# Optimization experiments

Hardware: AMD Instinct MI355X
Metric: run time of the kernel (lower is better)

The kernel has to match this reference:

```python
import jax, jax.numpy as jnp
import numpy as np

N_NODES = 100000
N_EDGES = 1600000
DIM = 64


def setup_inputs() -> dict:
    key = jax.random.key(0)
    k = jax.random.split(key, 7)
    x = jax.random.normal(k[0], (N_NODES, DIM), dtype=jnp.float32)
    edge_index = jax.random.randint(k[1], (2, N_EDGES), 0, N_NODES, dtype=jnp.int64)
    sim_weight = jax.random.uniform(k[2], (N_EDGES,), dtype=jnp.float32)
    rep = jax.random.normal(k[3], (N_NODES,), dtype=jnp.float32)
    node_signal = jax.random.uniform(k[4], (N_NODES,), dtype=jnp.float32)
    # xavier-normal-ish linear weights, stored as [in, out] for x @ W
    std = float(np.sqrt(2.0 / (DIM + DIM)))
    W = jax.random.normal(k[5], (DIM, DIM), dtype=jnp.float32) * std
    W_self = jax.random.normal(k[6], (DIM, DIM), dtype=jnp.float32) * std
    return {"x": x, "edge_index": edge_index, "sim_weight": sim_weight,
            "rep": rep, "node_signal": node_signal, "W": W, "W_self": W_self}


def reference(x, edge_index, sim_weight, rep, node_signal, W, W_self):
    row, col = edge_index[0], edge_index[1]
    n = x.shape[0]
    hx = x @ W                                   # [N, D]
    h_j = hx[col]                                # [E, D] gather
    gate = jax.nn.sigmoid(rep[row] + rep[col])   # [E]
    coef = sim_weight * gate * node_signal[col]  # [E] fused edge scalar
    msg = coef[:, None] * h_j                    # [E, D]
    out = jax.ops.segment_sum(msg, row, num_segments=n)              # [N, D]
    deg = jax.ops.segment_sum(jnp.ones_like(row, dtype=x.dtype), row,
                              num_segments=n)                        # [N]
    out = out / (deg[:, None] + 1e-6)
    out = out + jax.nn.sigmoid(rep)[:, None] * (x @ W_self)
    return jax.nn.leaky_relu(out, negative_slope=0.01)
```

## Files before the change

### kernel.cpp

```cpp
#include <hip/hip_runtime.h>
#include <math.h>

#define DIM 64
#define R_SHIFT 7
#define R_PART  128
#define CHUNK   2048
#define EPT     4
#define CAP     4096
#define PCAP    3072

static __device__ inline unsigned short f32_to_bf16(float f) {
    unsigned u = __float_as_uint(f);
    u += 0x7FFFu + ((u >> 16) & 1u);
    return (unsigned short)(u >> 16);
}
static __device__ inline float bf16_to_f32(unsigned short h) {
    return __uint_as_float((unsigned)h << 16);
}

static __device__ inline unsigned pack_entry(int c, float coef) {
    unsigned u = __float_as_uint(coef);
    u += 0x7FFFu + ((u >> 16) & 1u);
    unsigned cb = (u >> 16) & 0x7FFFu;
    return ((unsigned)c << 15) | cb;
}
static __device__ inline int entry_col(unsigned e) { return (int)(e >> 15); }
static __device__ inline float entry_coef(unsigned e) {
    return __uint_as_float((e & 0x7FFFu) << 16);
}

__global__ __launch_bounds__(256) void gemm_dual_tiled(
        const float* __restrict__ x,
        const float* __restrict__ W,
        const float* __restrict__ Wself,
        const float* __restrict__ rep,
        unsigned short* __restrict__ hxb,
        unsigned short* __restrict__ selfb, int n) {
    __shared__ float xs[64][68];
    __shared__ float Ws[64][64];
    __shared__ float Vs[64][64];

    const int t = threadIdx.x;
    const int row0 = blockIdx.x * 64;

    {
        const float4* W4 = (const float4*)W;
        const float4* V4 = (const float4*)Wself;
        float4* Ws4 = (float4*)&Ws[0][0];
        float4* Vs4 = (float4*)&Vs[0][0];
        for (int i = t; i < 1024; i += 256) { Ws4[i] = W4[i]; Vs4[i] = V4[i]; }
    }
    for (int i = t; i < 1024; i += 256) {
        int r = i >> 4, c4 = i & 15;
        float4 v = make_float4(0.f, 0.f, 0.f, 0.f);
        if (row0 + r < n) v = ((const float4*)x)[(size_t)(row0 + r) * 16 + c4];
        *(float4*)&xs[r][c4 * 4] = v;
    }
    __syncthreads();

    const int r0 = (t >> 4) * 4;
    const int c0 = (t & 15) * 4;

    float4 a1[4], a2[4];
#pragma unroll
    for (int j = 0; j < 4; ++j) {
        a1[j] = make_float4(0.f, 0.f, 0.f, 0.f);
        a2[j] = make_float4(0.f, 0.f, 0.f, 0.f);
    }

#pragma unroll 8
    for (int k = 0; k < 64; ++k) {
        float4 wv = *(const float4*)&Ws[k][c0];
        float4 vv = *(const float4*)&Vs[k][c0];
        float xk0 = xs[r0 + 0][k];
        float xk1 = xs[r0 + 1][k];
        float xk2 = xs[r0 + 2][k];
        float xk3 = xs[r0 + 3][k];

        a1[0].x = fmaf(xk0, wv.x, a1[0].x); a1[0].y = fmaf(xk0, wv.y, a1[0].y);
        a1[0].z = fmaf(xk0, wv.z, a1[0].z); a1[0].w = fmaf(xk0, wv.w, a1[0].w);
        a1[1].x = fmaf(xk1, wv.x, a1[1].x); a1[1].y = fmaf(xk1, wv.y, a1[1].y);
        a1[1].z = fmaf(xk1, wv.z, a1[1].z); a1[1].w = fmaf(xk1, wv.w, a1[1].w);
        a1[2].x = fmaf(xk2, wv.x, a1[2].x); a1[2].y = fmaf(xk2, wv.y, a1[2].y);
        a1[2].z = fmaf(xk2, wv.z, a1[2].z); a1[2].w = fmaf(xk2, wv.w, a1[2].w);
        a1[3].x = fmaf(xk3, wv.x, a1[3].x); a1[3].y = fmaf(xk3, wv.y, a1[3].y);
        a1[3].z = fmaf(xk3, wv.z, a1[3].z); a1[3].w = fmaf(xk3, wv.w, a1[3].w);

        a2[0].x = fmaf(xk0, vv.x, a2[0].x); a2[0].y = fmaf(xk0, vv.y, a2[0].y);
        a2[0].z = fmaf(xk0, vv.z, a2[0].z); a2[0].w = fmaf(xk0, vv.w, a2[0].w);
        a2[1].x = fmaf(xk1, vv.x, a2[1].x); a2[1].y = fmaf(xk1, vv.y, a2[1].y);
        a2[1].z = fmaf(xk1, vv.z, a2[1].z); a2[1].w = fmaf(xk1, vv.w, a2[1].w);
        a2[2].x = fmaf(xk2, vv.x, a2[2].x); a2[2].y = fmaf(xk2, vv.y, a2[2].y);
        a2[2].z = fmaf(xk2, vv.z, a2[2].z); a2[2].w = fmaf(xk2, vv.w, a2[2].w);
        a2[3].x = fmaf(xk3, vv.x, a2[3].x); a2[3].y = fmaf(xk3, vv.y, a2[3].y);
        a2[3].z = fmaf(xk3, vv.z, a2[3].z); a2[3].w = fmaf(xk3, vv.w, a2[3].w);
    }

#pragma unroll
    for (int j = 0; j < 4; ++j) {
        int row = row0 + r0 + j;
        if (row >= n) break;
        ushort4 hb;
        hb.x = f32_to_bf16(a1[j].x); hb.y = f32_to_bf16(a1[j].y);
        hb.z = f32_to_bf16(a1[j].z); hb.w = f32_to_bf16(a1[j].w);
        *(ushort4*)&hxb[(size_t)row * DIM + c0] = hb;
        float srep = 1.0f / (1.0f + __expf(-rep[row]));
        ushort4 sb;
        sb.x = f32_to_bf16(srep * a2[j].x); sb.y = f32_to_bf16(srep * a2[j].y);
        sb.z = f32_to_bf16(srep * a2[j].z); sb.w = f32_to_bf16(srep * a2[j].w);
        *(ushort4*)&selfb[(size_t)row * DIM + c0] = sb;
    }
}

__global__ __launch_bounds__(512) void ppart_kernel(
        const int* __restrict__ ei,
        const float* __restrict__ sw,
        const float* __restrict__ rep,
        const float* __restrict__ ns,
        int* __restrict__ pcur,
        uint2* __restrict__ tmp, int E, int NP) {
    __shared__ int cnt[1024];
    __shared__ int gb[1024];
    for (int p = threadIdx.x; p < NP; p += 512) cnt[p] = 0;
    __syncthreads();

    const int base = blockIdx.x * CHUNK;

    int r_[EPT], c_[EPT]; float sw_[EPT];
#pragma unroll
    for (int i = 0; i < EPT; ++i) {
        int e = base + i * 512 + threadIdx.x;
        bool v = (e < E);
        r_[i]  = v ? ei[e] : -1;
        c_[i]  = v ? ei[E + e] : 0;
        sw_[i] = v ? sw[e] : 0.f;
    }

    float repr[EPT], repc[EPT], nsc[EPT];
#pragma unroll
    for (int i = 0; i < EPT; ++i) {
        int rr = (r_[i] >= 0) ? r_[i] : 0;
        int cc = c_[i];
        repr[i] = rep[rr];
        repc[i] = rep[cc];
        nsc[i]  = ns[cc];
    }

    int pid[EPT]; int rank[EPT]; unsigned pay[EPT];
#pragma unroll
    for (int i = 0; i < EPT; ++i) {
        pid[i] = -1;
        if (r_[i] >= 0) {
            float gate = 1.0f / (1.0f + __expf(-(repr[i] + repc[i])));
            float coef = sw_[i] * gate * nsc[i];
            pid[i]  = r_[i] >> R_SHIFT;
            pay[i]  = pack_entry(c_[i], coef);
            rank[i] = atomicAdd(&cnt[pid[i]], 1);
        }
    }
    __syncthreads();

    for (int p = threadIdx.x; p < NP; p += 512) {
        int c = cnt[p];
        gb[p] = c ? atomicAdd(&pcur[p], c) : 0;
    }
    __syncthreads();

#pragma unroll
    for (int i = 0; i < EPT; ++i)
        if (pid[i] >= 0) {
            int s = gb[pid[i]] + rank[i];
            if (s < PCAP)
                tmp[(size_t)pid[i] * PCAP + s] = make_uint2((unsigned)r_[i], pay[i]);
        }
}

template<int K>
__device__ inline void lgather_k(const unsigned* __restrict__ sorted, int j,
                                 const unsigned short* __restrict__ hxb,
                                 int lane, float& acc) {
    unsigned e[K]; unsigned short h[K];
#pragma unroll
    for (int i = 0; i < K; ++i) e[i] = sorted[j + i];
#pragma unroll
    for (int i = 0; i < K; ++i) h[i] = hxb[(size_t)entry_col(e[i]) * DIM + lane];
#pragma unroll
    for (int i = 0; i < K; ++i) acc = fmaf(entry_coef(e[i]), bf16_to_f32(h[i]), acc);
}

__global__ __launch_bounds__(512) void pgather2_kernel(
        const int* __restrict__ pcur,
        const uint2* __restrict__ tmp,
        const unsigned short* __restrict__ hxb,
        const unsigned short* __restrict__ selfb,
        float* __restrict__ out, int n) {
    __shared__ unsigned sorted[CAP];
    __shared__ int rbase[R_PART + 1];
    __shared__ int rcnt[R_PART];
    __shared__ int rcur[R_PART];

    const int p   = blockIdx.x;
    const int tid = threadIdx.x;
    const size_t start = (size_t)p * PCAP;
    int cnt = pcur[p];
    if (cnt > PCAP) cnt = PCAP;

    if (tid < R_PART) rcnt[tid] = 0;
    __syncthreads();

    for (int i = tid; i < cnt; i += 512)
        atomicAdd(&rcnt[tmp[start + i].x & (R_PART - 1)], 1);
    __syncthreads();

    if (tid < 64) {
        int c0 = rcnt[2 * tid], c1 = rcnt[2 * tid + 1];
        int s = c0 + c1;
        int inc = s;
#pragma unroll
        for (int off = 1; off < 64; off <<= 1) {
            int t = __shfl_up(inc, off, 64);
            if (tid >= off) inc += t;
        }
        int excl = inc - s;
        rbase[2 * tid]     = excl;
        rbase[2 * tid + 1] = excl + c0;
        rcur[2 * tid]      = excl;
        rcur[2 * tid + 1]  = excl + c0;
        if (tid == 63) rbase[R_PART] = inc;
    }
    __syncthreads();

    for (int i = tid; i < cnt; i += 512) {
        uint2 t = tmp[start + i];
        int slot = atomicAdd(&rcur[t.x & (R_PART - 1)], 1);
        sorted[slot] = t.y;
    }
    __syncthreads();

    const int lane = tid & 63;
    const int w    = tid >> 6;
    const int gbase = p << R_SHIFT;
    for (int r = w; r < R_PART; r += 8) {
        int g = gbase + r;
        if (g >= n) continue;
        const int b0 = rbase[r], b1 = rbase[r + 1];
        float acc = 0.0f;
        int j = b0;
        for (; j + 8 <= b1; j += 8) lgather_k<8>(sorted, j, hxb, lane, acc);
        if (j + 4 <= b1) { lgather_k<4>(sorted, j, hxb, lane, acc); j += 4; }
        if (j + 2 <= b1) { lgather_k<2>(sorted, j, hxb, lane, acc); j += 2; }
        if (j < b1)      { lgather_k<1>(sorted, j, hxb, lane, acc); }

        float d = (float)(b1 - b0);
        float self = bf16_to_f32(selfb[(size_t)g * DIM + lane]);
        float v = acc / (d + 1e-6f) + self;
        out[(size_t)g * DIM + lane] = (v > 0.f) ? v : 0.01f * v;
    }
}

__global__ void gemm64_kernel(const float* __restrict__ x,
                              const float* __restrict__ W,
                              float* __restrict__ hx, int n) {
    __shared__ float Ws[DIM * DIM];
    for (int i = threadIdx.x; i < DIM * DIM; i += blockDim.x) Ws[i] = W[i];
    __syncthreads();
    const int lane = threadIdx.x & 63;
    const int wave = threadIdx.x >> 6;
    const int wpb  = blockDim.x >> 6;
    for (int row = blockIdx.x * wpb + wave; row < n; row += gridDim.x * wpb) {
        float xv = x[(size_t)row * DIM + lane];
        float acc = 0.0f;
#pragma unroll
        for (int k = 0; k < 64; ++k)
            acc = fmaf(__shfl(xv, k, 64), Ws[k * DIM + lane], acc);
        hx[(size_t)row * DIM + lane] = acc;
    }
}

__global__ void edge_scatter_kernel(const int* __restrict__ ei,
                                    const float* __restrict__ sw,
                                    const float* __restrict__ rep,
                                    const float* __restrict__ ns,
                                    const float* __restrict__ hx,
                                    float* __restrict__ out,
                                    float* __restrict__ deg, int E) {
    long long t = (long long)blockIdx.x * blockDim.x + threadIdx.x;
    int e = (int)(t >> 6);
    int d = (int)(t & 63);
    if (e >= E) return;
    int r = ei[e];
    int c = ei[E + e];
    float gate = 1.0f / (1.0f + __expf(-(rep[r] + rep[c])));
    float coef = sw[e] * gate * ns[c];
    atomicAdd(&out[(size_t)r * DIM + d], coef * hx[(size_t)c * DIM + d]);
    if (d == 0) atomicAdd(&deg[r], 1.0f);
}

__global__ void finalize_kernel(const float* __restrict__ x,
                                const float* __restrict__ Wself,
                                const float* __restrict__ rep,
                                const float* __restrict__ deg,
                                float* __restrict__ out, int n) {
    __shared__ float Ws[DIM * DIM];
    for (int i = threadIdx.x; i < DIM * DIM; i += blockDim.x) Ws[i] = Wself[i];
    __syncthreads();
    const int lane = threadIdx.x & 63;
    const int wave = threadIdx.x >> 6;
    const int wpb  = blockDim.x >> 6;
    for (int row = blockIdx.x * wpb + wave; row < n; row += gridDim.x * wpb) {
        float xv = x[(size_t)row * DIM + lane];
        float self = 0.0f;
#pragma unroll
        for (int k = 0; k < 64; ++k)
            self = fmaf(__shfl(xv, k, 64), Ws[k * DIM + lane], self);
        float srep = 1.0f / (1.0f + __expf(-rep[row]));
        float v = out[(size_t)row * DIM + lane] / (deg[row] + 1e-6f) + srep * self;
        out[(size_t)row * DIM + lane] = (v > 0.0f) ? v : 0.01f * v;
    }
}

extern "C" void kernel_launch(void* const* d_in, const int* in_sizes, int n_in,
                              void* d_out, int out_size, void* d_ws, size_t ws_size,
                              hipStream_t stream) {
    const float* x     = (const float*)d_in[0];
    const int*   ei    = (const int*)d_in[1];
    const float* sw    = (const float*)d_in[2];
    const float* rep   = (const float*)d_in[3];
    const float* ns    = (const float*)d_in[4];
    const float* W     = (const float*)d_in[5];
    const float* Wself = (const float*)d_in[6];

    const int n = in_sizes[0] / DIM;
    const int E = in_sizes[2];

    float* out = (float*)d_out;
    char*  ws  = (char*)d_ws;

    const int NP = (n + R_PART - 1) >> R_SHIFT;

    size_t off = 0;
    unsigned short* hxb   = (unsigned short*)(ws + off); off += (size_t)n * DIM * 2;
    unsigned short* selfb = (unsigned short*)(ws + off); off += (size_t)n * DIM * 2;
    uint2* tmp   = (uint2*)(ws + off); off += (size_t)NP * PCAP * 8;
    int*   pcur  = (int*)(ws + off);   off += (size_t)NP * 4;
    const size_t need = off;

    const int NBLK = (E + CHUNK - 1) / CHUNK;

    if (ws_size >= need && NP <= 1024) {
        hipMemsetAsync(pcur, 0, (size_t)NP * sizeof(int), stream);

        gemm_dual_tiled<<<(n + 63) / 64, 256, 0, stream>>>(
            x, W, Wself, rep, hxb, selfb, n);

        ppart_kernel<<<NBLK, 512, 0, stream>>>(ei, sw, rep, ns, pcur, tmp, E, NP);

        pgather2_kernel<<<NP, 512, 0, stream>>>(pcur, tmp, hxb, selfb, out, n);
    } else {
        float* hx2 = (float*)ws;
        float* deg = (float*)ws + (size_t)n * DIM;
        hipMemsetAsync(d_out, 0, (size_t)out_size * sizeof(float), stream);
        hipMemsetAsync(deg, 0, (size_t)n * sizeof(float), stream);
        {
            const int block = 256, wpb = block / 64;
            gemm64_kernel<<<(n + wpb - 1) / wpb, block, 0, stream>>>(x, W, hx2, n);
        }
        {
            long long total = (long long)E * DIM;
            edge_scatter_kernel<<<(int)((total + 255) / 256), 256, 0, stream>>>(
                ei, sw, rep, ns, hx2, out, deg, E);
        }
        {
            const int block = 256, wpb = block / 64;
            finalize_kernel<<<(n + wpb - 1) / wpb, block, 0, stream>>>(
                x, Wself, rep, deg, out, n);
        }
    }
}
```

Before: 126.5 us.

## Store hx and edge coefficients as fp8 e4m3 and pack edges into 32 bits

Converts the gathered hx rows from bf16 to a custom fp8 e4m3 encoding and packs each edge (local row, column, fp8 coefficient) into one 32-bit word instead of a uint2. A combined rep/node_signal float2 array is built in the GEMM kernel so each edge's column-side loads become one 8-byte read. These changes cut gather and partition-buffer traffic, at the cost of much coarser precision (3-bit mantissa, flush of small values), which may violate tolerance. Column indices are limited to 17 bits.

Result: slower. 149.5 us (+18.2%).

```diff
diff --git a/kernel.cpp b/kernel.cpp
--- a/kernel.cpp
+++ b/kernel.cpp
@@ -18,24 +18,39 @@
     return __uint_as_float((unsigned)h << 16);
 }
 
-static __device__ inline unsigned pack_entry(int c, float coef) {
-    unsigned u = __float_as_uint(coef);
-    u += 0x7FFFu + ((u >> 16) & 1u);
-    unsigned cb = (u >> 16) & 0x7FFFu;
-    return ((unsigned)c << 15) | cb;
-}
-static __device__ inline int entry_col(unsigned e) { return (int)(e >> 15); }
-static __device__ inline float entry_coef(unsigned e) {
-    return __uint_as_float((e & 0x7FFFu) << 16);
-}
+static __device__ inline unsigned f32_to_e4m3(float f) {
+    unsigned u = __float_as_uint(f);
+    unsigned s = (u >> 24) & 0x80u;
+    unsigned mag = u & 0x7FFFFFFFu;
+    if (mag < 0x3C800000u) return s;
+    if (mag >= 0x43E80000u) return s | 0x7Eu;
+    unsigned r = mag + 0x000FFFFFu + ((mag >> 20) & 1u);
+    return s | ((r >> 20) - 960u);
+}
+static __device__ inline float e4m3_to_f32(unsigned v) {
+    unsigned em = v & 0x7Fu;
+    unsigned s = (v & 0x80u) << 24;
+    unsigned f = em ? (s | ((em + 960u) << 20)) : s;
+    return __uint_as_float(f);
+}
+
+static __device__ inline unsigned pack_entry4(int r, int c, float coef) {
+    return ((unsigned)(r & (R_PART - 1)) << 25) | ((unsigned)c << 8)
+         | f32_to_e4m3(coef);
+}
+static __device__ inline int e_row(unsigned e)  { return (int)(e >> 25); }
+static __device__ inline int e_col(unsigned e)  { return (int)((e >> 8) & 0x1FFFFu); }
+static __device__ inline float e_coef(unsigned e) { return e4m3_to_f32(e & 0xFFu); }
 
 __global__ __launch_bounds__(256) void gemm_dual_tiled(
         const float* __restrict__ x,
         const float* __restrict__ W,
         const float* __restrict__ Wself,
         const float* __restrict__ rep,
-        unsigned short* __restrict__ hxb,
-        unsigned short* __restrict__ selfb, int n) {
+        const float* __restrict__ ns,
+        unsigned char* __restrict__ hxb8,
+        unsigned short* __restrict__ selfb,
+        float2* __restrict__ repns, int n) {
     __shared__ float xs[64][68];
     __shared__ float Ws[64][64];
     __shared__ float Vs[64][64];
@@ -55,6 +70,10 @@
         float4 v = make_float4(0.f, 0.f, 0.f, 0.f);
         if (row0 + r < n) v = ((const float4*)x)[(size_t)(row0 + r) * 16 + c4];
         *(float4*)&xs[r][c4 * 4] = v;
+    }
+    if (t < 64) {
+        int row = row0 + t;
+        if (row < n) repns[row] = make_float2(rep[row], ns[row]);
     }
     __syncthreads();
 
@@ -100,10 +119,12 @@
     for (int j = 0; j < 4; ++j) {
         int row = row0 + r0 + j;
         if (row >= n) break;
-        ushort4 hb;
-        hb.x = f32_to_bf16(a1[j].x); hb.y = f32_to_bf16(a1[j].y);
-        hb.z = f32_to_bf16(a1[j].z); hb.w = f32_to_bf16(a1[j].w);
-        *(ushort4*)&hxb[(size_t)row * DIM + c0] = hb;
+        uchar4 h8;
+        h8.x = (unsigned char)f32_to_e4m3(a1[j].x);
+        h8.y = (unsigned char)f32_to_e4m3(a1[j].y);
+        h8.z = (unsigned char)f32_to_e4m3(a1[j].z);
+        h8.w = (unsigned char)f32_to_e4m3(a1[j].w);
+        *(uchar4*)&hxb8[(size_t)row * DIM + c0] = h8;
         float srep = 1.0f / (1.0f + __expf(-rep[row]));
         ushort4 sb;
         sb.x = f32_to_bf16(srep * a2[j].x); sb.y = f32_to_bf16(srep * a2[j].y);
@@ -116,9 +137,9 @@
         const int* __restrict__ ei,
         const float* __restrict__ sw,
         const float* __restrict__ rep,
-        const float* __restrict__ ns,
+        const float2* __restrict__ repns,
         int* __restrict__ pcur,
-        uint2* __restrict__ tmp, int E, int NP) {
+        unsigned* __restrict__ tmp, int E, int NP) {
     __shared__ int cnt[1024];
     __shared__ int gb[1024];
     for (int p = threadIdx.x; p < NP; p += 512) cnt[p] = 0;
@@ -136,14 +157,12 @@
         sw_[i] = v ? sw[e] : 0.f;
     }
 
-    float repr[EPT], repc[EPT], nsc[EPT];
+    float repr[EPT]; float2 rn[EPT];
 #pragma unroll
     for (int i = 0; i < EPT; ++i) {
         int rr = (r_[i] >= 0) ? r_[i] : 0;
-        int cc = c_[i];
         repr[i] = rep[rr];
-        repc[i] = rep[cc];
-        nsc[i]  = ns[cc];
+        rn[i]   = repns[c_[i]];
     }
 
     int pid[EPT]; int rank[EPT]; unsigned pay[EPT];
@@ -151,10 +170,10 @@
     for (int i = 0; i < EPT; ++i) {
         pid[i] = -1;
         if (r_[i] >= 0) {
-            float gate = 1.0f / (1.0f + __expf(-(repr[i] + repc[i])));
-            float coef = sw_[i] * gate * nsc[i];
+            float gate = 1.0f / (1.0f + __expf(-(repr[i] + rn[i].x)));
+            float coef = sw_[i] * gate * rn[i].y;
             pid[i]  = r_[i] >> R_SHIFT;
-            pay[i]  = pack_entry(c_[i], coef);
+            pay[i]  = pack_entry4(r_[i], c_[i], coef);
             rank[i] = atomicAdd(&cnt[pid[i]], 1);
         }
     }
@@ -171,27 +190,28 @@
         if (pid[i] >= 0) {
             int s = gb[pid[i]] + rank[i];
             if (s < PCAP)
-                tmp[(size_t)pid[i] * PCAP + s] = make_uint2((unsigned)r_[i], pay[i]);
+                tmp[(size_t)pid[i] * PCAP + s] = pay[i];
         }
 }
 
 template<int K>
 __device__ inline void lgather_k(const unsigned* __restrict__ sorted, int j,
-                                 const unsigned short* __restrict__ hxb,
+                                 const unsigned char* __restrict__ hxb8,
                                  int lane, float& acc) {
-    unsigned e[K]; unsigned short h[K];
+    unsigned e[K]; unsigned char h[K];
 #pragma unroll
     for (int i = 0; i < K; ++i) e[i] = sorted[j + i];
 #pragma unroll
-    for (int i = 0; i < K; ++i) h[i] = hxb[(size_t)entry_col(e[i]) * DIM + lane];
-#pragma unroll
-    for (int i = 0; i < K; ++i) acc = fmaf(entry_coef(e[i]), bf16_to_f32(h[i]), acc);
+    for (int i = 0; i < K; ++i) h[i] = hxb8[(size_t)e_col(e[i]) * DIM + lane];
+#pragma unroll
+    for (int i = 0; i < K; ++i)
+        acc = fmaf(e_coef(e[i]), e4m3_to_f32(h[i]), acc);
 }
 
 __global__ __launch_bounds__(512) void pgather2_kernel(
         const int* __restrict__ pcur,
-        const uint2* __restrict__ tmp,
-        const unsigned short* __restrict__ hxb,
+        const unsigned* __restrict__ tmp,
+        const unsigned char* __restrict__ hxb8,
         const unsigned short* __restrict__ selfb,
         float* __restrict__ out, int n) {
     __shared__ unsigned sorted[CAP];
@@ -209,7 +229,7 @@
     __syncthreads();
 
     for (int i = tid; i < cnt; i += 512)
-        atomicAdd(&rcnt[tmp[start + i].x & (R_PART - 1)], 1);
+        atomicAdd(&rcnt[tmp[start + i] >> 25], 1);
     __syncthreads();
 
     if (tid < 64) {
@@ -231,9 +251,9 @@
     __syncthreads();
 
     for (int i = tid; i < cnt; i += 512) {
-        uint2 t = tmp[start + i];
-        int slot = atomicAdd(&rcur[t.x & (R_PART - 1)], 1);
-        sorted[slot] = t.y;
+        unsigned e = tmp[start + i];
+        int slot = atomicAdd(&rcur[e >> 25], 1);
+        sorted[slot] = e;
     }
     __syncthreads();
 
@@ -246,10 +266,10 @@
         const int b0 = rbase[r], b1 = rbase[r + 1];
         float acc = 0.0f;
         int j = b0;
-        for (; j + 8 <= b1; j += 8) lgather_k<8>(sorted, j, hxb, lane, acc);
-        if (j + 4 <= b1) { lgather_k<4>(sorted, j, hxb, lane, acc); j += 4; }
-        if (j + 2 <= b1) { lgather_k<2>(sorted, j, hxb, lane, acc); j += 2; }
-        if (j < b1)      { lgather_k<1>(sorted, j, hxb, lane, acc); }
+        for (; j + 8 <= b1; j += 8) lgather_k<8>(sorted, j, hxb8, lane, acc);
+        if (j + 4 <= b1) { lgather_k<4>(sorted, j, hxb8, lane, acc); j += 4; }
+        if (j + 2 <= b1) { lgather_k<2>(sorted, j, hxb8, lane, acc); j += 2; }
+        if (j < b1)      { lgather_k<1>(sorted, j, hxb8, lane, acc); }
 
         float d = (float)(b1 - b0);
         float self = bf16_to_f32(selfb[(size_t)g * DIM + lane]);
@@ -339,9 +359,10 @@
     const int NP = (n + R_PART - 1) >> R_SHIFT;
 
     size_t off = 0;
-    unsigned short* hxb   = (unsigned short*)(ws + off); off += (size_t)n * DIM * 2;
+    unsigned char*  hxb8  = (unsigned char*)(ws + off);  off += (size_t)n * DIM;
     unsigned short* selfb = (unsigned short*)(ws + off); off += (size_t)n * DIM * 2;
-    uint2* tmp   = (uint2*)(ws + off); off += (size_t)NP * PCAP * 8;
+    float2* repns = (float2*)(ws + off); off += (size_t)n * 8;
+    unsigned* tmp = (unsigned*)(ws + off); off += (size_t)NP * PCAP * 4;
     int*   pcur  = (int*)(ws + off);   off += (size_t)NP * 4;
     const size_t need = off;
 
@@ -351,11 +372,11 @@
         hipMemsetAsync(pcur, 0, (size_t)NP * sizeof(int), stream);
 
         gemm_dual_tiled<<<(n + 63) / 64, 256, 0, stream>>>(
-            x, W, Wself, rep, hxb, selfb, n);
-
-        ppart_kernel<<<NBLK, 512, 0, stream>>>(ei, sw, rep, ns, pcur, tmp, E, NP);
-
-        pgather2_kernel<<<NP, 512, 0, stream>>>(pcur, tmp, hxb, selfb, out, n);
+            x, W, Wself, rep, ns, hxb8, selfb, repns, n);
+
+        ppart_kernel<<<NBLK, 512, 0, stream>>>(ei, sw, rep, repns, pcur, tmp, E, NP);
+
+        pgather2_kernel<<<NP, 512, 0, stream>>>(pcur, tmp, hxb8, selfb, out, n);
     } else {
         float* hx2 = (float*)ws;
         float* deg = (float*)ws + (size_t)n * DIM;
```
